# Optimization experiments

Hardware: AMD Instinct MI355X
Metric: run time of the kernel (lower is better)

## Reference

```python
import jax, jax.numpy as jnp
import numpy as np

DIM = 1280
NUM_HEADS = 16
HEAD_DIM = DIM // NUM_HEADS  # 80
HIDDEN = DIM * 4             # 5120
SEQ = 4096
EPS = 1e-6


def _layernorm(x, scale, bias):
    mu = jnp.mean(x, axis=-1, keepdims=True)
    var = jnp.mean((x - mu) ** 2, axis=-1, keepdims=True)
    return (x - mu) * jax.lax.rsqrt(var + EPS) * scale + bias


def _rotate_half(x):
    x1, x2 = jnp.split(x, 2, axis=-1)
    return jnp.concatenate([-x2, x1], axis=-1)


def _apply_rope(x, freqs):
    # x: [N, H, D], freqs: [N, D//2]
    orig = x.dtype
    x = x.astype(jnp.float32)
    cos = jnp.repeat(jnp.cos(freqs), 2, axis=-1)[:, None, :].astype(jnp.float32)  # [N,1,D]
    sin = jnp.repeat(jnp.sin(freqs), 2, axis=-1)[:, None, :].astype(jnp.float32)
    return (x * cos + _rotate_half(x) * sin).astype(orig)


def _quick_gelu(x):
    return x * jax.nn.sigmoid(1.702 * x)


def setup_inputs() -> dict:
    key = jax.random.key(0)
    ks = jax.random.split(key, 12)
    s = 0.02
    inp = {
        "hidden_states": jax.random.normal(ks[0], (SEQ, DIM), dtype=jnp.float32),
        "rotary_pos_emb": jax.random.normal(ks[1], (SEQ, HEAD_DIM // 2), dtype=jnp.float32),
        "cu_seqlens": jnp.array([0, 1024, 2048, 3072, 4096], dtype=jnp.int32),
        "w_qkv": jax.random.normal(ks[2], (DIM, 3 * DIM), dtype=jnp.float32) * s,
        "b_qkv": jnp.zeros((3 * DIM,), dtype=jnp.float32),
        "w_proj": jax.random.normal(ks[3], (DIM, DIM), dtype=jnp.float32) * s,
        "b_proj": jnp.zeros((DIM,), dtype=jnp.float32),
        "w_fc1": jax.random.normal(ks[4], (DIM, HIDDEN), dtype=jnp.float32) * s,
        "b_fc1": jnp.zeros((HIDDEN,), dtype=jnp.float32),
        "w_fc2": jax.random.normal(ks[5], (HIDDEN, DIM), dtype=jnp.float32) * s,
        "b_fc2": jnp.zeros((DIM,), dtype=jnp.float32),
        "ln1_scale": jnp.ones((DIM,), dtype=jnp.float32),
        "ln1_bias": jnp.zeros((DIM,), dtype=jnp.float32),
        "ln2_scale": jnp.ones((DIM,), dtype=jnp.float32),
        "ln2_bias": jnp.zeros((DIM,), dtype=jnp.float32),
    }
    return inp


def _attention(x, cu_seqlens, rotary_pos_emb, w_qkv, b_qkv, w_proj, b_proj):
    N = x.shape[0]
    qkv = (x @ w_qkv + b_qkv).reshape(N, 3, NUM_HEADS, HEAD_DIM)
    q, k, v = qkv[:, 0], qkv[:, 1], qkv[:, 2]  # each [N, H, D]
    q = _apply_rope(q, rotary_pos_emb)
    k = _apply_rope(k, rotary_pos_emb)
    # block-diagonal mask from cu_seqlens (faithful to original construction)
    row_ids = jnp.arange(N)[None, None, :]
    col_ids = jnp.arange(N)[None, :, None]
    starts = cu_seqlens[:-1][:, None, None]
    ends = cu_seqlens[1:][:, None, None]
    is_valid = (row_ids >= starts) & (row_ids < ends) & (col_ids >= starts) & (col_ids < ends)
    combined = jnp.any(is_valid, axis=0)  # [N, N]
    bias = jnp.where(combined, 0.0, jnp.finfo(q.dtype).min)
    scores = jnp.einsum("shd,thd->hst", q, k) / np.sqrt(HEAD_DIM).astype(np.float32)
    scores = scores + bias[None, :, :]
    probs = jax.nn.softmax(scores.astype(jnp.float32), axis=-1).astype(q.dtype)
    out = jnp.einsum("hst,thd->shd", probs, v).reshape(N, DIM)
    return out @ w_proj + b_proj


def reference(hidden_states, rotary_pos_emb, cu_seqlens, w_qkv, b_qkv, w_proj, b_proj,
              w_fc1, b_fc1, w_fc2, b_fc2, ln1_scale, ln1_bias, ln2_scale, ln2_bias):
    h = hidden_states
    h = h + _attention(_layernorm(h, ln1_scale, ln1_bias), cu_seqlens, rotary_pos_emb,
                       w_qkv, b_qkv, w_proj, b_proj)
    m = _layernorm(h, ln2_scale, ln2_bias)
    h = h + (_quick_gelu(m @ w_fc1 + b_fc1) @ w_fc2 + b_fc2)
    return h
```

## Files before the change

kernel.cpp:

```cpp
#include <hip/hip_runtime.h>
#include <hip/hip_bf16.h>
#include <math.h>

typedef __bf16 bf16;
typedef __bf16 bf16x8 __attribute__((ext_vector_type(8)));
typedef float f32x4 __attribute__((ext_vector_type(4)));

#define DIM 1280
#define SEQ 4096
#define NH 16
#define HD 80
#define HIDDEN 5120
#define FLAG_THRESH 4096

#define S_VMCNT(n) asm volatile("s_waitcnt vmcnt(" #n ")" ::: "memory")
#define S_BAR() __builtin_amdgcn_s_barrier()

__device__ __forceinline__ void gl_lds16(const bf16* g, bf16* l) {
  __builtin_amdgcn_global_load_lds((const __attribute__((address_space(1))) void*)g,
                                   (__attribute__((address_space(3))) void*)l, 16, 0, 0);
}

__device__ __forceinline__ f32x4 fz4() { f32x4 v; v.x = 0.f; v.y = 0.f; v.z = 0.f; v.w = 0.f; return v; }

__device__ __forceinline__ float ldx(const void* p, size_t i, bool f32) {
  if (f32) return ((const float*)p)[i];
  return (float)((const bf16*)p)[i];
}

__global__ void zero_flag_k(int* flag) { *flag = 0; }

__global__ __launch_bounds__(256) void sniff_k(const unsigned short* h, int n, int* flag) {
  int i = blockIdx.x * 256 + threadIdx.x;
  int c = 0;
  for (int idx = i; idx < n; idx += 256 * gridDim.x) {
    int e = (h[idx] >> 7) & 0xFF;
    c += (e >= 0xC8) ? 1 : 0;
  }
  #pragma unroll
  for (int o = 32; o; o >>= 1) c += __shfl_down(c, o);
  if ((threadIdx.x & 63) == 0 && c) atomicAdd(flag, c);
}

__global__ __launch_bounds__(256) void transpose_k(const void* __restrict__ in, bf16* __restrict__ out,
                                                   int R, int C, const int* __restrict__ flag) {
  bool f32 = *flag > FLAG_THRESH;
  __shared__ bf16 tile[32][33];
  int c0 = blockIdx.x * 32, r0 = blockIdx.y * 32;
  int tx = threadIdx.x, ty = threadIdx.y;
  #pragma unroll
  for (int i = 0; i < 4; i++)
    tile[ty + 8 * i][tx] = (bf16)ldx(in, (size_t)(r0 + ty + 8 * i) * C + c0 + tx, f32);
  __syncthreads();
  #pragma unroll
  for (int i = 0; i < 4; i++)
    out[(size_t)(c0 + ty + 8 * i) * R + r0 + tx] = tile[tx][ty + 8 * i];
}

__global__ __launch_bounds__(256) void ln_k(const void* __restrict__ x, const void* __restrict__ sc,
                                            const void* __restrict__ bi, bf16* __restrict__ out,
                                            const int* __restrict__ flag, int force_f32) {
  bool pf32 = *flag > FLAG_THRESH;
  bool xf32 = force_f32 || pf32;
  int row = blockIdx.x, t = threadIdx.x;
  float v[5];
  float s = 0.f, sq = 0.f;
  #pragma unroll
  for (int i = 0; i < 5; i++) {
    v[i] = ldx(x, (size_t)row * DIM + i * 256 + t, xf32);
    s += v[i]; sq += v[i] * v[i];
  }
  #pragma unroll
  for (int o = 32; o; o >>= 1) { s += __shfl_down(s, o); sq += __shfl_down(sq, o); }
  __shared__ float rs[4], rq[4];
  if ((t & 63) == 0) { rs[t >> 6] = s; rq[t >> 6] = sq; }
  __syncthreads();
  s = rs[0] + rs[1] + rs[2] + rs[3];
  sq = rq[0] + rq[1] + rq[2] + rq[3];
  float mean = s * (1.f / DIM);
  float var = sq * (1.f / DIM) - mean * mean;
  float rstd = rsqrtf(fmaxf(var, 0.f) + 1e-6f);
  #pragma unroll
  for (int i = 0; i < 5; i++) {
    int c = i * 256 + t;
    out[(size_t)row * DIM + c] = (bf16)((v[i] - mean) * rstd * ldx(sc, c, pf32) + ldx(bi, c, pf32));
  }
}

template <int TN>
__device__ __forceinline__ void gemm_step(const bf16* As, const bf16* Bs, f32x4 (&acc)[4][TN],
                                          int wm, int wn, int quad, int l15) {
  bf16x8 af[4], bfr[TN];
  #pragma unroll
  for (int tm = 0; tm < 4; tm++) af[tm] = *(const bf16x8*)&As[(wm + tm * 16 + l15) * 32 + quad * 8];
  #pragma unroll
  for (int tn = 0; tn < TN; tn++) bfr[tn] = *(const bf16x8*)&Bs[(wn + tn * 16 + l15) * 32 + quad * 8];
  #pragma unroll
  for (int tm = 0; tm < 4; tm++)
    #pragma unroll
    for (int tn = 0; tn < TN; tn++)
      acc[tm][tn] = __builtin_amdgcn_mfma_f32_16x16x32_bf16(af[tm], bfr[tn], acc[tm][tn], 0, 0, 0);
}

template <int MODE, int NT>
__global__ __launch_bounds__(256) void gemm_bt(const bf16* __restrict__ A, const bf16* __restrict__ Bt,
                                               const void* __restrict__ bias, const void* __restrict__ res,
                                               void* __restrict__ out, int M, int N, int K,
                                               const int* __restrict__ flag) {
  bool pf32 = *flag > FLAG_THRESH;
  constexpr int TN = NT / 32;
  __shared__ bf16 As0[128 * 32];
  __shared__ bf16 As1[128 * 32];
  __shared__ bf16 Bs0[NT * 32];
  __shared__ bf16 Bs1[NT * 32];
  int tid = threadIdx.x;
  int lane = tid & 63, wv = tid >> 6;
  int quad = lane >> 4, l15 = lane & 15;
  int m0 = blockIdx.y * 128, n0 = blockIdx.x * NT;
  int wm = (wv & 1) * 64, wn = (wv >> 1) * (NT / 2);
  const bf16* Ag = A + (size_t)m0 * K;
  const bf16* Bg = Bt + (size_t)n0 * K;
  int r0 = tid >> 2, c0 = (tid & 3) * 8;
  int r1 = r0 + 64;
  f32x4 acc[4][TN];
  #pragma unroll
  for (int i = 0; i < 4; i++)
    #pragma unroll
    for (int j = 0; j < TN; j++) acc[i][j] = fz4();

#define STAGE_BT(as, bs, kk) do {                                        \
    gl_lds16(Ag + (size_t)r0 * K + (kk) + c0, &(as)[tid * 8]);           \
    gl_lds16(Ag + (size_t)r1 * K + (kk) + c0, &(as)[(tid + 256) * 8]);   \
    gl_lds16(Bg + (size_t)r0 * K + (kk) + c0, &(bs)[tid * 8]);           \
    if constexpr (NT == 128) gl_lds16(Bg + (size_t)r1 * K + (kk) + c0, &(bs)[(tid + 256) * 8]); \
  } while (0)

  STAGE_BT(As0, Bs0, 0);
  for (int k0 = 0; k0 < K; k0 += 64) {
    STAGE_BT(As1, Bs1, k0 + 32);
    if constexpr (NT == 128) { S_VMCNT(4); } else { S_VMCNT(3); }
    S_BAR();
    gemm_step<TN>(As0, Bs0, acc, wm, wn, quad, l15);
    S_BAR();
    if (k0 + 64 < K) {
      STAGE_BT(As0, Bs0, k0 + 64);
      if constexpr (NT == 128) { S_VMCNT(4); } else { S_VMCNT(3); }
    } else {
      S_VMCNT(0);
    }
    S_BAR();
    gemm_step<TN>(As1, Bs1, acc, wm, wn, quad, l15);
    S_BAR();
  }
#undef STAGE_BT

  #pragma unroll
  for (int tm = 0; tm < 4; tm++) {
    #pragma unroll
    for (int tn = 0; tn < TN; tn++) {
      #pragma unroll
      for (int r = 0; r < 4; r++) {
        int row = m0 + wm + tm * 16 + quad * 4 + r;
        int col = n0 + wn + tn * 16 + l15;
        size_t idx = (size_t)row * N + col;
        float vv = acc[tm][tn][r] + ldx(bias, col, pf32);
        if constexpr (MODE == 0) ((bf16*)out)[idx] = (bf16)vv;
        if constexpr (MODE == 1) ((float*)out)[idx] = vv + ldx(res, idx, pf32);
        if constexpr (MODE == 2) ((bf16*)out)[idx] = (bf16)(vv / (1.f + __expf(-1.702f * vv)));
      }
    }
  }
}

__global__ __launch_bounds__(256) void gemm_sk(const bf16* __restrict__ A, const bf16* __restrict__ Bt,
                                               float* __restrict__ part, int M, int N, int K, int chunk) {
  __shared__ bf16 As0[128 * 32];
  __shared__ bf16 As1[128 * 32];
  __shared__ bf16 Bs0[64 * 32];
  __shared__ bf16 Bs1[64 * 32];
  int tid = threadIdx.x;
  int lane = tid & 63, wv = tid >> 6;
  int quad = lane >> 4, l15 = lane & 15;
  int m0 = blockIdx.y * 128, n0 = blockIdx.x * 64;
  int wm = (wv & 1) * 64, wn = (wv >> 1) * 32;
  int kb = blockIdx.z * chunk;
  const bf16* Ag = A + (size_t)m0 * K;
  const bf16* Bg = Bt + (size_t)n0 * K;
  int r0 = tid >> 2, c0 = (tid & 3) * 8;
  int r1 = r0 + 64;
  f32x4 acc[4][2];
  #pragma unroll
  for (int i = 0; i < 4; i++)
    #pragma unroll
    for (int j = 0; j < 2; j++) acc[i][j] = fz4();

#define STAGE_SK(as, bs, kk) do {                                        \
    gl_lds16(Ag + (size_t)r0 * K + (kk) + c0, &(as)[tid * 8]);           \
    gl_lds16(Ag + (size_t)r1 * K + (kk) + c0, &(as)[(tid + 256) * 8]);   \
    gl_lds16(Bg + (size_t)r0 * K + (kk) + c0, &(bs)[tid * 8]);           \
  } while (0)

  STAGE_SK(As0, Bs0, kb);
  for (int k0 = kb; k0 < kb + chunk; k0 += 64) {
    STAGE_SK(As1, Bs1, k0 + 32);
    S_VMCNT(3);
    S_BAR();
    gemm_step<2>(As0, Bs0, acc, wm, wn, quad, l15);
    S_BAR();
    if (k0 + 64 < kb + chunk) {
      STAGE_SK(As0, Bs0, k0 + 64);
      S_VMCNT(3);
    } else {
      S_VMCNT(0);
    }
    S_BAR();
    gemm_step<2>(As1, Bs1, acc, wm, wn, quad, l15);
    S_BAR();
  }
#undef STAGE_SK

  float* po = part + (size_t)blockIdx.z * M * N;
  #pragma unroll
  for (int tm = 0; tm < 4; tm++) {
    #pragma unroll
    for (int tn = 0; tn < 2; tn++) {
      #pragma unroll
      for (int r = 0; r < 4; r++) {
        int row = m0 + wm + tm * 16 + quad * 4 + r;
        int col = n0 + wn + tn * 16 + l15;
        po[(size_t)row * N + col] = acc[tm][tn][r];
      }
    }
  }
}

__global__ __launch_bounds__(256) void reduce2_k(const float* __restrict__ p0, const float* __restrict__ p1,
                                                 const void* __restrict__ bias, const float* __restrict__ res,
                                                 float* __restrict__ out, int NCOL,
                                                 const int* __restrict__ flag) {
  bool pf32 = *flag > FLAG_THRESH;
  size_t i = ((size_t)blockIdx.x * 256 + threadIdx.x) * 4;
  int col = (int)(i % NCOL);
  float4 a = *(const float4*)&p0[i];
  float4 b = *(const float4*)&p1[i];
  float4 r = *(const float4*)&res[i];
  float4 o;
  o.x = a.x + b.x + r.x + ldx(bias, col + 0, pf32);
  o.y = a.y + b.y + r.y + ldx(bias, col + 1, pf32);
  o.z = a.z + b.z + r.z + ldx(bias, col + 2, pf32);
  o.w = a.w + b.w + r.w + ldx(bias, col + 3, pf32);
  *(float4*)&out[i] = o;
}

__global__ __launch_bounds__(256) void rope_k(bf16* __restrict__ qkv, const void* __restrict__ rot,
                                              const int* __restrict__ flag) {
  bool pf32 = *flag > FLAG_THRESH;
  int idx = blockIdx.x * 256 + threadIdx.x;
  int d = idx % 40;
  int t = idx / 40;
  int head = t & 15;
  int seq = t >> 4;
  float f1 = ldx(rot, (size_t)seq * 40 + (d >> 1), pf32);
  float f2 = ldx(rot, (size_t)seq * 40 + (d >> 1) + 20, pf32);
  float c1 = cosf(f1), s1 = sinf(f1), c2 = cosf(f2), s2 = sinf(f2);
  const float scq = 0.11180339887498949f;
  size_t base = (size_t)seq * (3 * DIM) + head * HD + d;
  float x1 = (float)qkv[base], x2 = (float)qkv[base + 40];
  qkv[base] = (bf16)((x1 * c1 - x2 * s1) * scq);
  qkv[base + 40] = (bf16)((x2 * c2 + x1 * s2) * scq);
  x1 = (float)qkv[base + DIM]; x2 = (float)qkv[base + DIM + 40];
  qkv[base + DIM] = (bf16)(x1 * c1 - x2 * s1);
  qkv[base + DIM + 40] = (bf16)(x2 * c2 + x1 * s2);
}

__global__ __launch_bounds__(256, 4) void attn_k(const bf16* __restrict__ qkv, const int* __restrict__ cu,
                                                 bf16* __restrict__ out) {
  __shared__ __align__(16) char smem[38144];
  bf16* Qs = (bf16*)smem;
  bf16* Ks = (bf16*)(smem + 13312);
  bf16* Vt = (bf16*)(smem + 26624);
  bf16* Ps = (bf16*)smem;
  int tid = threadIdx.x, lane = tid & 63, wv = tid >> 6;
  int quad = lane >> 4, l15 = lane & 15;
  int qt = blockIdx.x, head = blockIdx.y, seg = blockIdx.z;
  int s0 = cu[seg], s1 = cu[seg + 1];
  int q0 = s0 + qt * 64;
  if (q0 >= s1) return;
  const bf16* qh = qkv + head * HD;
  const bf16* kh = qkv + DIM + head * HD;
  const bf16* vh = qkv + 2 * DIM + head * HD;
  const int RS = 3 * DIM;
  uint4 z4; z4.x = 0; z4.y = 0; z4.z = 0; z4.w = 0;
  for (int i = tid; i < 128; i += 256) {
    int r = i >> 1, c = i & 1;
    *(uint4*)&Qs[r * 104 + 80 + c * 8] = z4;
    *(uint4*)&Ks[r * 104 + 80 + c * 8] = z4;
  }
  for (int i = tid; i < 640; i += 256) {
    int r = i / 10, c = i % 10;
    *(bf16x8*)&Qs[r * 104 + c * 8] = *(const bf16x8*)&qh[(size_t)(q0 + r) * RS + c * 8];
  }
  __syncthreads();
  bf16x8 aq[3];
  #pragma unroll
  for (int ks = 0; ks < 3; ks++)
    aq[ks] = *(const bf16x8*)&Qs[(wv * 16 + l15) * 104 + ks * 32 + quad * 8];

  float m_r[4], l_r[4];
  f32x4 oacc[5];
  #pragma unroll
  for (int r = 0; r < 4; r++) { m_r[r] = -1e30f; l_r[r] = 0.f; }
  #pragma unroll
  for (int nt = 0; nt < 5; nt++) oacc[nt] = fz4();

  for (int kt = s0; kt < s1; kt += 64) {
    __syncthreads();
    for (int i = tid; i < 640; i += 256) {
      int r = i / 10, c = i % 10;
      *(bf16x8*)&Ks[r * 104 + c * 8] = *(const bf16x8*)&kh[(size_t)(kt + r) * RS + c * 8];
    }
    for (int i = tid; i < 640; i += 256) {
      int c = i >> 6, r = i & 63;
      bf16x8 vv = *(const bf16x8*)&vh[(size_t)(kt + r) * RS + c * 8];
      #pragma unroll
      for (int j = 0; j < 8; j++) Vt[(c * 8 + j) * 72 + r] = vv[j];
    }
    __syncthreads();
    f32x4 sacc[4];
    #pragma unroll
    for (int j = 0; j < 4; j++) sacc[j] = fz4();
    __builtin_amdgcn_s_setprio(1);
    #pragma unroll
    for (int ks = 0; ks < 3; ks++) {
      #pragma unroll
      for (int j = 0; j < 4; j++) {
        bf16x8 bk = *(const bf16x8*)&Ks[(j * 16 + l15) * 104 + ks * 32 + quad * 8];
        sacc[j] = __builtin_amdgcn_mfma_f32_16x16x32_bf16(aq[ks], bk, sacc[j], 0, 0, 0);
      }
    }
    __builtin_amdgcn_s_setprio(0);
    #pragma unroll
    for (int r = 0; r < 4; r++) {
      float mx = fmaxf(fmaxf(sacc[0][r], sacc[1][r]), fmaxf(sacc[2][r], sacc[3][r]));
      #pragma unroll
      for (int o = 8; o; o >>= 1) mx = fmaxf(mx, __shfl_xor(mx, o));
      float mnew = fmaxf(m_r[r], mx);
      float alpha = __expf(m_r[r] - mnew);
      float psum = 0.f;
      #pragma unroll
      for (int j = 0; j < 4; j++) {
        float p = __expf(sacc[j][r] - mnew);
        psum += p;
        Ps[wv * 1152 + (quad * 4 + r) * 72 + j * 16 + l15] = (bf16)p;
      }
      #pragma unroll
      for (int o = 8; o; o >>= 1) psum += __shfl_xor(psum, o);
      l_r[r] = l_r[r] * alpha + psum;
      m_r[r] = mnew;
      #pragma unroll
      for (int nt = 0; nt < 5; nt++) oacc[nt][r] *= alpha;
    }
    __builtin_amdgcn_s_setprio(1);
    #pragma unroll
    for (int ks = 0; ks < 2; ks++) {
      bf16x8 ap = *(const bf16x8*)&Ps[wv * 1152 + l15 * 72 + ks * 32 + quad * 8];
      #pragma unroll
      for (int nt = 0; nt < 5; nt++) {
        bf16x8 bv = *(const bf16x8*)&Vt[(nt * 16 + l15) * 72 + ks * 32 + quad * 8];
        oacc[nt] = __builtin_amdgcn_mfma_f32_16x16x32_bf16(ap, bv, oacc[nt], 0, 0, 0);
      }
    }
    __builtin_amdgcn_s_setprio(0);
  }
  #pragma unroll
  for (int nt = 0; nt < 5; nt++) {
    #pragma unroll
    for (int r = 0; r < 4; r++) {
      int row = q0 + wv * 16 + quad * 4 + r;
      int d = nt * 16 + l15;
      out[(size_t)row * DIM + head * HD + d] = (bf16)(oacc[nt][r] / l_r[r]);
    }
  }
}

#define FLAG_OFF 0UL
#define QKVT_OFF 256UL
#define PROJT_OFF 9830656UL
#define FC1T_OFF 13107456UL
#define FC2T_OFF 26214656UL
#define LN_OFF 39321856UL
#define QKV_OFF 49807616UL
#define PART_OFF 49807616UL
#define AO_OFF 81264896UL
#define H1_OFF 91750656UL
#define FC1O_OFF 112722176UL

extern "C" void kernel_launch(void* const* d_in, const int* in_sizes, int n_in,
                              void* d_out, int out_size, void* d_ws, size_t ws_size,
                              hipStream_t stream) {
  const void* hidden = d_in[0];
  const void* rot    = d_in[1];
  const int*  cu     = (const int*)d_in[2];
  const void* w_qkv  = d_in[3];
  const void* b_qkv  = d_in[4];
  const void* w_proj = d_in[5];
  const void* b_proj = d_in[6];
  const void* w_fc1  = d_in[7];
  const void* b_fc1  = d_in[8];
  const void* w_fc2  = d_in[9];
  const void* b_fc2  = d_in[10];
  const void* ln1s   = d_in[11];
  const void* ln1b   = d_in[12];
  const void* ln2s   = d_in[13];
  const void* ln2b   = d_in[14];

  char* ws = (char*)d_ws;
  int* flag   = (int*)(ws + FLAG_OFF);
  bf16* qkvT  = (bf16*)(ws + QKVT_OFF);
  bf16* projT = (bf16*)(ws + PROJT_OFF);
  bf16* fc1T  = (bf16*)(ws + FC1T_OFF);
  bf16* fc2T  = (bf16*)(ws + FC2T_OFF);
  bf16* ln_bf = (bf16*)(ws + LN_OFF);
  bf16* qkv   = (bf16*)(ws + QKV_OFF);
  float* part = (float*)(ws + PART_OFF);
  bf16* ao    = (bf16*)(ws + AO_OFF);
  float* h1   = (float*)(ws + H1_OFF);
  bf16* fc1o  = (bf16*)(ws + FC1O_OFF);

  zero_flag_k<<<1, 1, 0, stream>>>(flag);
  sniff_k<<<256, 256, 0, stream>>>((const unsigned short*)hidden, SEQ * DIM, flag);

  dim3 tb(32, 8);
  transpose_k<<<dim3(120, 40), tb, 0, stream>>>(w_qkv, qkvT, 1280, 3840, flag);
  transpose_k<<<dim3(40, 40), tb, 0, stream>>>(w_proj, projT, 1280, 1280, flag);
  transpose_k<<<dim3(160, 40), tb, 0, stream>>>(w_fc1, fc1T, 1280, 5120, flag);
  transpose_k<<<dim3(40, 160), tb, 0, stream>>>(w_fc2, fc2T, 5120, 1280, flag);

  ln_k<<<SEQ, 256, 0, stream>>>(hidden, ln1s, ln1b, ln_bf, flag, 0);
  gemm_bt<0, 128><<<dim3(30, 32), 256, 0, stream>>>(ln_bf, qkvT, b_qkv, nullptr, qkv, SEQ, 3 * DIM, DIM, flag);
  rope_k<<<10240, 256, 0, stream>>>(qkv, rot, flag);
  attn_k<<<dim3(16, NH, 4), 256, 0, stream>>>(qkv, cu, ao);
  gemm_bt<1, 64><<<dim3(20, 32), 256, 0, stream>>>(ao, projT, b_proj, hidden, h1, SEQ, DIM, DIM, flag);
  ln_k<<<SEQ, 256, 0, stream>>>(h1, ln2s, ln2b, ln_bf, flag, 1);
  gemm_bt<2, 128><<<dim3(40, 32), 256, 0, stream>>>(ln_bf, fc1T, b_fc1, nullptr, fc1o, SEQ, HIDDEN, DIM, flag);
  gemm_sk<<<dim3(20, 32, 2), 256, 0, stream>>>(fc1o, fc2T, part, SEQ, DIM, HIDDEN, HIDDEN / 2);
  reduce2_k<<<SEQ * DIM / 1024, 256, 0, stream>>>(part, part + (size_t)SEQ * DIM, b_fc2, h1,
                                                  (float*)d_out, DIM, flag);
}
```

Before: 656.5 us.

## Replace GEMMs with 256x256-tile, 4-stage pipelined, LDS-swizzled MFMA kernel

Adds a gemm256 kernel with 256x256 output tiles, 512 threads (8 waves, each computing 128x64), a 4-deep global_load_lds ring buffer, an XOR swizzle on LDS columns to reduce bank conflicts, and s_setprio around the MFMA block. It replaces the 128-row gemm_bt kernels for the QKV, projection and FC1 GEMMs, keeping the same epilogues. The goal is more data reuse per LDS byte and better hiding of load latency. In exchange, the 128KB of LDS allows only one block per CU, and the grids shrink to 240, 80 and 320 blocks. That leaves the projection GEMM underfilling the CUs and gives FC1 a tail wave.

```diff
diff --git a/kernel.cpp b/kernel.cpp
--- a/kernel.cpp
+++ b/kernel.cpp
@@ -15,6 +15,7 @@
 
 #define S_VMCNT(n) asm volatile("s_waitcnt vmcnt(" #n ")" ::: "memory")
 #define S_BAR() __builtin_amdgcn_s_barrier()
+#define SCHED0() __builtin_amdgcn_sched_barrier(0)
 
 __device__ __forceinline__ void gl_lds16(const bf16* g, bf16* l) {
   __builtin_amdgcn_global_load_lds((const __attribute__((address_space(1))) void*)g,
@@ -87,6 +88,86 @@
   }
 }
 
+template <int MODE>
+__global__ __launch_bounds__(512, 2) void gemm256(const bf16* __restrict__ A, const bf16* __restrict__ Bt,
+                                                  const void* __restrict__ bias, const void* __restrict__ res,
+                                                  void* __restrict__ out, int M, int N, int K,
+                                                  const int* __restrict__ flag) {
+  bool pf32 = *flag > FLAG_THRESH;
+  __shared__ bf16 As[4][256 * 32];
+  __shared__ bf16 Bs[4][256 * 32];
+  int tid = threadIdx.x;
+  int lane = tid & 63;
+  int wv = tid >> 6;
+  int quad = lane >> 4, l15 = lane & 15;
+  int wm = wv >> 2, wn = wv & 3;
+  int m0 = blockIdx.y * 256, n0 = blockIdx.x * 256;
+  const bf16* Ag = A + (size_t)m0 * K;
+  const bf16* Bg = Bt + (size_t)n0 * K;
+  int r0 = tid >> 2;
+  int r1 = r0 + 128;
+  int c0s = (((tid & 3) ^ ((tid >> 3) & 3))) * 8;
+  int sq8 = (quad ^ ((l15 >> 1) & 3)) * 8;
+
+  f32x4 acc[8][4];
+  #pragma unroll
+  for (int i = 0; i < 8; i++)
+    #pragma unroll
+    for (int j = 0; j < 4; j++) acc[i][j] = fz4();
+
+#define STG256(s) do { int _sl = (s) & 3; size_t _k = (size_t)(s) * 32;          \
+    gl_lds16(Ag + (size_t)r0 * K + _k + c0s, &As[_sl][tid * 8]);                 \
+    gl_lds16(Ag + (size_t)r1 * K + _k + c0s, &As[_sl][(tid + 512) * 8]);         \
+    gl_lds16(Bg + (size_t)r0 * K + _k + c0s, &Bs[_sl][tid * 8]);                 \
+    gl_lds16(Bg + (size_t)r1 * K + _k + c0s, &Bs[_sl][(tid + 512) * 8]); } while (0)
+
+#define CMP256(p) do { const bf16* _A = As[(p) & 3]; const bf16* _B = Bs[(p) & 3];          \
+    bf16x8 af[8], bfr[4];                                                                   \
+    _Pragma("unroll")                                                                       \
+    for (int mi = 0; mi < 8; mi++) af[mi] = *(const bf16x8*)&_A[(wm * 128 + mi * 16 + l15) * 32 + sq8]; \
+    _Pragma("unroll")                                                                       \
+    for (int ni = 0; ni < 4; ni++) bfr[ni] = *(const bf16x8*)&_B[(wn * 64 + ni * 16 + l15) * 32 + sq8]; \
+    __builtin_amdgcn_s_setprio(1);                                                          \
+    _Pragma("unroll")                                                                       \
+    for (int mi = 0; mi < 8; mi++)                                                          \
+      _Pragma("unroll")                                                                     \
+      for (int ni = 0; ni < 4; ni++)                                                        \
+        acc[mi][ni] = __builtin_amdgcn_mfma_f32_16x16x32_bf16(af[mi], bfr[ni], acc[mi][ni], 0, 0, 0); \
+    __builtin_amdgcn_s_setprio(0); } while (0)
+
+  int NS = K >> 5;
+  STG256(0); STG256(1); STG256(2);
+  for (int p = 0; p < NS - 2; ++p) {
+    S_VMCNT(8);
+    S_BAR();
+    SCHED0();
+    if (p + 3 < NS) STG256(p + 3);
+    CMP256(p);
+  }
+  S_VMCNT(4); S_BAR(); SCHED0(); CMP256(NS - 2);
+  S_VMCNT(0); S_BAR(); SCHED0(); CMP256(NS - 1);
+#undef STG256
+#undef CMP256
+
+  #pragma unroll
+  for (int ni = 0; ni < 4; ni++) {
+    int col = n0 + wn * 64 + ni * 16 + l15;
+    float bv = ldx(bias, col, pf32);
+    #pragma unroll
+    for (int mi = 0; mi < 8; mi++) {
+      #pragma unroll
+      for (int r = 0; r < 4; r++) {
+        int row = m0 + wm * 128 + mi * 16 + quad * 4 + r;
+        size_t idx = (size_t)row * N + col;
+        float vv = acc[mi][ni][r] + bv;
+        if constexpr (MODE == 0) ((bf16*)out)[idx] = (bf16)vv;
+        if constexpr (MODE == 1) ((float*)out)[idx] = vv + ldx(res, idx, pf32);
+        if constexpr (MODE == 2) ((bf16*)out)[idx] = (bf16)(vv / (1.f + __expf(-1.702f * vv)));
+      }
+    }
+  }
+}
+
 template <int TN>
 __device__ __forceinline__ void gemm_step(const bf16* As, const bf16* Bs, f32x4 (&acc)[4][TN],
                                           int wm, int wn, int quad, int l15) {
@@ -100,76 +181,6 @@
     #pragma unroll
     for (int tn = 0; tn < TN; tn++)
       acc[tm][tn] = __builtin_amdgcn_mfma_f32_16x16x32_bf16(af[tm], bfr[tn], acc[tm][tn], 0, 0, 0);
-}
-
-template <int MODE, int NT>
-__global__ __launch_bounds__(256) void gemm_bt(const bf16* __restrict__ A, const bf16* __restrict__ Bt,
-                                               const void* __restrict__ bias, const void* __restrict__ res,
-                                               void* __restrict__ out, int M, int N, int K,
-                                               const int* __restrict__ flag) {
-  bool pf32 = *flag > FLAG_THRESH;
-  constexpr int TN = NT / 32;
-  __shared__ bf16 As0[128 * 32];
-  __shared__ bf16 As1[128 * 32];
-  __shared__ bf16 Bs0[NT * 32];
-  __shared__ bf16 Bs1[NT * 32];
-  int tid = threadIdx.x;
-  int lane = tid & 63, wv = tid >> 6;
-  int quad = lane >> 4, l15 = lane & 15;
-  int m0 = blockIdx.y * 128, n0 = blockIdx.x * NT;
-  int wm = (wv & 1) * 64, wn = (wv >> 1) * (NT / 2);
-  const bf16* Ag = A + (size_t)m0 * K;
-  const bf16* Bg = Bt + (size_t)n0 * K;
-  int r0 = tid >> 2, c0 = (tid & 3) * 8;
-  int r1 = r0 + 64;
-  f32x4 acc[4][TN];
-  #pragma unroll
-  for (int i = 0; i < 4; i++)
-    #pragma unroll
-    for (int j = 0; j < TN; j++) acc[i][j] = fz4();
-
-#define STAGE_BT(as, bs, kk) do {                                        \
-    gl_lds16(Ag + (size_t)r0 * K + (kk) + c0, &(as)[tid * 8]);           \
-    gl_lds16(Ag + (size_t)r1 * K + (kk) + c0, &(as)[(tid + 256) * 8]);   \
-    gl_lds16(Bg + (size_t)r0 * K + (kk) + c0, &(bs)[tid * 8]);           \
-    if constexpr (NT == 128) gl_lds16(Bg + (size_t)r1 * K + (kk) + c0, &(bs)[(tid + 256) * 8]); \
-  } while (0)
-
-  STAGE_BT(As0, Bs0, 0);
-  for (int k0 = 0; k0 < K; k0 += 64) {
-    STAGE_BT(As1, Bs1, k0 + 32);
-    if constexpr (NT == 128) { S_VMCNT(4); } else { S_VMCNT(3); }
-    S_BAR();
-    gemm_step<TN>(As0, Bs0, acc, wm, wn, quad, l15);
-    S_BAR();
-    if (k0 + 64 < K) {
-      STAGE_BT(As0, Bs0, k0 + 64);
-      if constexpr (NT == 128) { S_VMCNT(4); } else { S_VMCNT(3); }
-    } else {
-      S_VMCNT(0);
-    }
-    S_BAR();
-    gemm_step<TN>(As1, Bs1, acc, wm, wn, quad, l15);
-    S_BAR();
-  }
-#undef STAGE_BT
-
-  #pragma unroll
-  for (int tm = 0; tm < 4; tm++) {
-    #pragma unroll
-    for (int tn = 0; tn < TN; tn++) {
-      #pragma unroll
-      for (int r = 0; r < 4; r++) {
-        int row = m0 + wm + tm * 16 + quad * 4 + r;
-        int col = n0 + wn + tn * 16 + l15;
-        size_t idx = (size_t)row * N + col;
-        float vv = acc[tm][tn][r] + ldx(bias, col, pf32);
-        if constexpr (MODE == 0) ((bf16*)out)[idx] = (bf16)vv;
-        if constexpr (MODE == 1) ((float*)out)[idx] = vv + ldx(res, idx, pf32);
-        if constexpr (MODE == 2) ((bf16*)out)[idx] = (bf16)(vv / (1.f + __expf(-1.702f * vv)));
-      }
-    }
-  }
 }
 
 __global__ __launch_bounds__(256) void gemm_sk(const bf16* __restrict__ A, const bf16* __restrict__ Bt,
@@ -437,12 +448,12 @@
   transpose_k<<<dim3(40, 160), tb, 0, stream>>>(w_fc2, fc2T, 5120, 1280, flag);
 
   ln_k<<<SEQ, 256, 0, stream>>>(hidden, ln1s, ln1b, ln_bf, flag, 0);
-  gemm_bt<0, 128><<<dim3(30, 32), 256, 0, stream>>>(ln_bf, qkvT, b_qkv, nullptr, qkv, SEQ, 3 * DIM, DIM, flag);
+  gemm256<0><<<dim3(15, 16), 512, 0, stream>>>(ln_bf, qkvT, b_qkv, nullptr, qkv, SEQ, 3 * DIM, DIM, flag);
   rope_k<<<10240, 256, 0, stream>>>(qkv, rot, flag);
   attn_k<<<dim3(16, NH, 4), 256, 0, stream>>>(qkv, cu, ao);
-  gemm_bt<1, 64><<<dim3(20, 32), 256, 0, stream>>>(ao, projT, b_proj, hidden, h1, SEQ, DIM, DIM, flag);
+  gemm256<1><<<dim3(5, 16), 512, 0, stream>>>(ao, projT, b_proj, hidden, h1, SEQ, DIM, DIM, flag);
   ln_k<<<SEQ, 256, 0, stream>>>(h1, ln2s, ln2b, ln_bf, flag, 1);
-  gemm_bt<2, 128><<<dim3(40, 32), 256, 0, stream>>>(ln_bf, fc1T, b_fc1, nullptr, fc1o, SEQ, HIDDEN, DIM, flag);
+  gemm256<2><<<dim3(20, 16), 512, 0, stream>>>(ln_bf, fc1T, b_fc1, nullptr, fc1o, SEQ, HIDDEN, DIM, flag);
   gemm_sk<<<dim3(20, 32, 2), 256, 0, stream>>>(fc1o, fc2T, part, SEQ, DIM, HIDDEN, HIDDEN / 2);
   reduce2_k<<<SEQ * DIM / 1024, 256, 0, stream>>>(part, part + (size_t)SEQ * DIM, b_fc2, h1,
                                                   (float*)d_out, DIM, flag);
```

After: 723.2 us. 1.1x slower.

## Double GEMM K-tile to 64 with XOR-swizzled LDS layout

Applied to the files above, without the earlier changes.

The GEMM and split-K kernels now stage 64-wide K slices per buffer instead of 32, halving the number of barrier/wait rounds per K. The LDS layout gets an XOR swizzle on 16-byte column chunks, applied both in the global-to-LDS load and in the fragment reads, to avoid bank conflicts on the wider rows. LDS use doubles per block, which may lower occupancy. K (and split-K chunk) must now be a multiple of 128.

```diff
diff --git a/kernel.cpp b/kernel.cpp
--- a/kernel.cpp
+++ b/kernel.cpp
@@ -88,18 +88,23 @@
 }
 
 template <int TN>
-__device__ __forceinline__ void gemm_step(const bf16* As, const bf16* Bs, f32x4 (&acc)[4][TN],
-                                          int wm, int wn, int quad, int l15) {
-  bf16x8 af[4], bfr[TN];
-  #pragma unroll
-  for (int tm = 0; tm < 4; tm++) af[tm] = *(const bf16x8*)&As[(wm + tm * 16 + l15) * 32 + quad * 8];
-  #pragma unroll
-  for (int tn = 0; tn < TN; tn++) bfr[tn] = *(const bf16x8*)&Bs[(wn + tn * 16 + l15) * 32 + quad * 8];
-  #pragma unroll
-  for (int tm = 0; tm < 4; tm++)
-    #pragma unroll
-    for (int tn = 0; tn < TN; tn++)
-      acc[tm][tn] = __builtin_amdgcn_mfma_f32_16x16x32_bf16(af[tm], bfr[tn], acc[tm][tn], 0, 0, 0);
+__device__ __forceinline__ void gemm_step64(const bf16* As, const bf16* Bs, f32x4 (&acc)[4][TN],
+                                            int wm, int wn, int quad, int l15) {
+  int rsw = l15 & 7;
+  #pragma unroll
+  for (int ks = 0; ks < 2; ks++) {
+    int csw = ((ks * 4 + quad) ^ rsw) * 8;
+    bf16x8 af[4], bfr[TN];
+    #pragma unroll
+    for (int tm = 0; tm < 4; tm++) af[tm] = *(const bf16x8*)&As[(wm + tm * 16 + l15) * 64 + csw];
+    #pragma unroll
+    for (int tn = 0; tn < TN; tn++) bfr[tn] = *(const bf16x8*)&Bs[(wn + tn * 16 + l15) * 64 + csw];
+    #pragma unroll
+    for (int tm = 0; tm < 4; tm++)
+      #pragma unroll
+      for (int tn = 0; tn < TN; tn++)
+        acc[tm][tn] = __builtin_amdgcn_mfma_f32_16x16x32_bf16(af[tm], bfr[tn], acc[tm][tn], 0, 0, 0);
+  }
 }
 
 template <int MODE, int NT>
@@ -109,10 +114,11 @@
                                                const int* __restrict__ flag) {
   bool pf32 = *flag > FLAG_THRESH;
   constexpr int TN = NT / 32;
-  __shared__ bf16 As0[128 * 32];
-  __shared__ bf16 As1[128 * 32];
-  __shared__ bf16 Bs0[NT * 32];
-  __shared__ bf16 Bs1[NT * 32];
+  constexpr int NB = NT / 32;
+  __shared__ bf16 As0[128 * 64];
+  __shared__ bf16 As1[128 * 64];
+  __shared__ bf16 Bs0[NT * 64];
+  __shared__ bf16 Bs1[NT * 64];
   int tid = threadIdx.x;
   int lane = tid & 63, wv = tid >> 6;
   int quad = lane >> 4, l15 = lane & 15;
@@ -120,36 +126,38 @@
   int wm = (wv & 1) * 64, wn = (wv >> 1) * (NT / 2);
   const bf16* Ag = A + (size_t)m0 * K;
   const bf16* Bg = Bt + (size_t)n0 * K;
-  int r0 = tid >> 2, c0 = (tid & 3) * 8;
-  int r1 = r0 + 64;
+  int r0 = tid >> 3;
+  int c0s = ((tid & 7) ^ ((tid >> 3) & 7)) * 8;
   f32x4 acc[4][TN];
   #pragma unroll
   for (int i = 0; i < 4; i++)
     #pragma unroll
     for (int j = 0; j < TN; j++) acc[i][j] = fz4();
 
-#define STAGE_BT(as, bs, kk) do {                                        \
-    gl_lds16(Ag + (size_t)r0 * K + (kk) + c0, &(as)[tid * 8]);           \
-    gl_lds16(Ag + (size_t)r1 * K + (kk) + c0, &(as)[(tid + 256) * 8]);   \
-    gl_lds16(Bg + (size_t)r0 * K + (kk) + c0, &(bs)[tid * 8]);           \
-    if constexpr (NT == 128) gl_lds16(Bg + (size_t)r1 * K + (kk) + c0, &(bs)[(tid + 256) * 8]); \
+#define STAGE_BT(as, bs, kk) do {                                                          \
+    _Pragma("unroll")                                                                      \
+    for (int j = 0; j < 4; j++)                                                            \
+      gl_lds16(Ag + (size_t)(r0 + j * 32) * K + (kk) + c0s, &(as)[(tid + j * 256) * 8]);   \
+    _Pragma("unroll")                                                                      \
+    for (int j = 0; j < NB; j++)                                                           \
+      gl_lds16(Bg + (size_t)(r0 + j * 32) * K + (kk) + c0s, &(bs)[(tid + j * 256) * 8]);   \
   } while (0)
 
   STAGE_BT(As0, Bs0, 0);
-  for (int k0 = 0; k0 < K; k0 += 64) {
-    STAGE_BT(As1, Bs1, k0 + 32);
-    if constexpr (NT == 128) { S_VMCNT(4); } else { S_VMCNT(3); }
-    S_BAR();
-    gemm_step<TN>(As0, Bs0, acc, wm, wn, quad, l15);
-    S_BAR();
-    if (k0 + 64 < K) {
-      STAGE_BT(As0, Bs0, k0 + 64);
-      if constexpr (NT == 128) { S_VMCNT(4); } else { S_VMCNT(3); }
+  for (int k0 = 0; k0 < K; k0 += 128) {
+    STAGE_BT(As1, Bs1, k0 + 64);
+    if constexpr (NT == 128) { S_VMCNT(8); } else { S_VMCNT(6); }
+    S_BAR();
+    gemm_step64<TN>(As0, Bs0, acc, wm, wn, quad, l15);
+    S_BAR();
+    if (k0 + 128 < K) {
+      STAGE_BT(As0, Bs0, k0 + 128);
+      if constexpr (NT == 128) { S_VMCNT(8); } else { S_VMCNT(6); }
     } else {
       S_VMCNT(0);
     }
     S_BAR();
-    gemm_step<TN>(As1, Bs1, acc, wm, wn, quad, l15);
+    gemm_step64<TN>(As1, Bs1, acc, wm, wn, quad, l15);
     S_BAR();
   }
 #undef STAGE_BT
@@ -174,10 +182,10 @@
 
 __global__ __launch_bounds__(256) void gemm_sk(const bf16* __restrict__ A, const bf16* __restrict__ Bt,
                                                float* __restrict__ part, int M, int N, int K, int chunk) {
-  __shared__ bf16 As0[128 * 32];
-  __shared__ bf16 As1[128 * 32];
-  __shared__ bf16 Bs0[64 * 32];
-  __shared__ bf16 Bs1[64 * 32];
+  __shared__ bf16 As0[128 * 64];
+  __shared__ bf16 As1[128 * 64];
+  __shared__ bf16 Bs0[64 * 64];
+  __shared__ bf16 Bs1[64 * 64];
   int tid = threadIdx.x;
   int lane = tid & 63, wv = tid >> 6;
   int quad = lane >> 4, l15 = lane & 15;
@@ -186,35 +194,38 @@
   int kb = blockIdx.z * chunk;
   const bf16* Ag = A + (size_t)m0 * K;
   const bf16* Bg = Bt + (size_t)n0 * K;
-  int r0 = tid >> 2, c0 = (tid & 3) * 8;
-  int r1 = r0 + 64;
+  int r0 = tid >> 3;
+  int c0s = ((tid & 7) ^ ((tid >> 3) & 7)) * 8;
   f32x4 acc[4][2];
   #pragma unroll
   for (int i = 0; i < 4; i++)
     #pragma unroll
     for (int j = 0; j < 2; j++) acc[i][j] = fz4();
 
-#define STAGE_SK(as, bs, kk) do {                                        \
-    gl_lds16(Ag + (size_t)r0 * K + (kk) + c0, &(as)[tid * 8]);           \
-    gl_lds16(Ag + (size_t)r1 * K + (kk) + c0, &(as)[(tid + 256) * 8]);   \
-    gl_lds16(Bg + (size_t)r0 * K + (kk) + c0, &(bs)[tid * 8]);           \
+#define STAGE_SK(as, bs, kk) do {                                                          \
+    _Pragma("unroll")                                                                      \
+    for (int j = 0; j < 4; j++)                                                            \
+      gl_lds16(Ag + (size_t)(r0 + j * 32) * K + (kk) + c0s, &(as)[(tid + j * 256) * 8]);   \
+    _Pragma("unroll")                                                                      \
+    for (int j = 0; j < 2; j++)                                                            \
+      gl_lds16(Bg + (size_t)(r0 + j * 32) * K + (kk) + c0s, &(bs)[(tid + j * 256) * 8]);   \
   } while (0)
 
   STAGE_SK(As0, Bs0, kb);
-  for (int k0 = kb; k0 < kb + chunk; k0 += 64) {
-    STAGE_SK(As1, Bs1, k0 + 32);
-    S_VMCNT(3);
-    S_BAR();
-    gemm_step<2>(As0, Bs0, acc, wm, wn, quad, l15);
-    S_BAR();
-    if (k0 + 64 < kb + chunk) {
-      STAGE_SK(As0, Bs0, k0 + 64);
-      S_VMCNT(3);
+  for (int k0 = kb; k0 < kb + chunk; k0 += 128) {
+    STAGE_SK(As1, Bs1, k0 + 64);
+    S_VMCNT(6);
+    S_BAR();
+    gemm_step64<2>(As0, Bs0, acc, wm, wn, quad, l15);
+    S_BAR();
+    if (k0 + 128 < kb + chunk) {
+      STAGE_SK(As0, Bs0, k0 + 128);
+      S_VMCNT(6);
     } else {
       S_VMCNT(0);
     }
     S_BAR();
-    gemm_step<2>(As1, Bs1, acc, wm, wn, quad, l15);
+    gemm_step64<2>(As1, Bs1, acc, wm, wn, quad, l15);
     S_BAR();
   }
 #undef STAGE_SK
```

Result: faster. 606.6 us (-7.6%).
